# Kernel tuning notes

Hardware: AMD Instinct MI355X
Metric: run time of the kernel (lower is better)

The kernel has to match this reference:

```python
import jax, jax.numpy as jnp
import numpy as np

B, L, D, H = 8, 256, 512, 512
NEG_BIG = 1e8  # matches the 100000000.0 mask constant in the original


def setup_inputs() -> dict:
    key = jax.random.key(0)
    k1, k2, k3, k4 = jax.random.split(key, 4)
    enc = jax.random.normal(k1, (B, L, D), dtype=jnp.float32)
    # Glorot-uniform init, matching tf.keras.initializers.GlorotUniform
    s_w = float(np.sqrt(6.0 / (D + H)))
    W_l = jax.random.uniform(k2, (D, H), jnp.float32, -s_w, s_w)
    W_r = jax.random.uniform(k3, (D, H), jnp.float32, -s_w, s_w)
    s_u = float(np.sqrt(6.0 / (H + H)))  # 1-D glorot: fan_in = fan_out = H
    U = jax.random.uniform(k4, (H,), jnp.float32, -s_u, s_u)
    logit_bias = jnp.zeros((1,), jnp.float32)  # bias_initial_value=None -> zeros init
    return {"encoder_output": enc, "W_l": W_l, "W_r": W_r, "U": U, "logit_bias": logit_bias}


def reference(encoder_output, W_l, W_r, U, logit_bias):
    # dot_l[b,i,h], dot_r[b,j,h]
    dot_l = jnp.einsum('bik,kh->bih', encoder_output, W_l)
    dot_r = jnp.einsum('bjk,kh->bjh', encoder_output, W_r)
    # additive biaffine: tanh(dot_l_i + dot_r_j) . U  -> logits[b,i,j]
    final_sum = jnp.tanh(dot_l[:, :, None, :] + dot_r[:, None, :, :])  # [B,L,L,H]
    logits = jnp.einsum('bijh,h->bij', final_sum, U) + logit_bias[0]   # [B,L,L]
    # per-row self-mask (one_hot(i)) applied over all rows at once
    masked = logits - NEG_BIG * jnp.eye(L, dtype=logits.dtype)[None]   # [B,L,L]
    # original returns python lists over i of [B,L]; stack -> [L,B,L]
    mask_scores = jnp.transpose(masked, (1, 0, 2))
    p = jax.nn.sigmoid(mask_scores)
    samples = jax.random.bernoulli(jax.random.key(42), p).astype(jnp.int32)  # [L,B,L]
    # Bernoulli entropy from logits x: p*softplus(-x) + (1-p)*softplus(x)
    entropy = p * jax.nn.softplus(-mask_scores) + (1.0 - p) * jax.nn.softplus(mask_scores)
    return samples, mask_scores, entropy
```

## Files before the change

### kernel.cpp

```cpp
#include <hip/hip_runtime.h>
#include <stdint.h>

#define Bb 8
#define Ll 256
#define Dd 512
#define Hh 512
#define Nout (Ll * Bb * Ll)

#define Kc 2.8853900817779268

#define RNG_PARTITIONABLE 1

typedef __attribute__((ext_vector_type(8))) short bf16x8;
typedef __attribute__((ext_vector_type(4))) float f32x4;

__device__ __forceinline__ uint32_t rotl32(uint32_t v, int s) {
  return (v << s) | (v >> (32 - s));
}
__device__ __forceinline__ void tf_round(uint32_t& x0, uint32_t& x1, int r) {
  x0 += x1;
  x1 = rotl32(x1, r);
  x1 ^= x0;
}
__device__ __forceinline__ uint2 threefry2x32_k042(uint32_t x0, uint32_t x1) {
  const uint32_t k0 = 0u;
  const uint32_t k1 = 42u;
  const uint32_t k2 = 0x1BD11BDAu ^ k0 ^ k1;
  x0 += k0; x1 += k1;
  tf_round(x0, x1, 13); tf_round(x0, x1, 15); tf_round(x0, x1, 26); tf_round(x0, x1, 6);
  x0 += k1; x1 += k2 + 1u;
  tf_round(x0, x1, 17); tf_round(x0, x1, 29); tf_round(x0, x1, 16); tf_round(x0, x1, 24);
  x0 += k2; x1 += k0 + 2u;
  tf_round(x0, x1, 13); tf_round(x0, x1, 15); tf_round(x0, x1, 26); tf_round(x0, x1, 6);
  x0 += k0; x1 += k1 + 3u;
  tf_round(x0, x1, 17); tf_round(x0, x1, 29); tf_round(x0, x1, 16); tf_round(x0, x1, 24);
  x0 += k1; x1 += k2 + 4u;
  tf_round(x0, x1, 13); tf_round(x0, x1, 15); tf_round(x0, x1, 26); tf_round(x0, x1, 6);
  x0 += k2; x1 += k0 + 5u;
  return make_uint2(x0, x1);
}

__device__ __forceinline__ uint32_t rng_bits(uint32_t n) {
#if RNG_PARTITIONABLE
  uint2 o = threefry2x32_k042(0u, n);
  return o.x ^ o.y;
#else
  const uint32_t half = (uint32_t)(Nout / 2);
  if (n < half) {
    uint2 o = threefry2x32_k042(n, n + half);
    return o.x;
  } else {
    uint2 o = threefry2x32_k042(n - half, n);
    return o.y;
  }
#endif
}

__device__ __forceinline__ unsigned short bf16_rne(float f) {
  uint32_t u = __float_as_uint(f);
  u = (u + 0x7fffu + ((u >> 16) & 1u)) >> 16;
  return (unsigned short)u;
}
__device__ __forceinline__ float bf16_tof(unsigned short h) {
  return __uint_as_float(((uint32_t)h) << 16);
}
__device__ __forceinline__ void split3(float a, unsigned short& h,
                                       unsigned short& m, unsigned short& l) {
  h = bf16_rne(a);
  const float r1 = a - bf16_tof(h);
  m = bf16_rne(r1);
  const float r2 = r1 - bf16_tof(m);
  l = bf16_rne(r2);
}

__global__ __launch_bounds__(256) void split_enc(
    const float* __restrict__ enc, unsigned short* __restrict__ ah,
    unsigned short* __restrict__ am, unsigned short* __restrict__ al) {
  const int idx = (blockIdx.x * 256 + threadIdx.x) * 4;
  const float4 v = *(const float4*)(enc + idx);
  ushort4 h4, m4, l4;
  split3(v.x, h4.x, m4.x, l4.x);
  split3(v.y, h4.y, m4.y, l4.y);
  split3(v.z, h4.z, m4.z, l4.z);
  split3(v.w, h4.w, m4.w, l4.w);
  *(ushort4*)(ah + idx) = h4;
  *(ushort4*)(am + idx) = m4;
  *(ushort4*)(al + idx) = l4;
}

__global__ __launch_bounds__(256) void split_wt(
    const float* __restrict__ Wl, const float* __restrict__ Wr,
    unsigned short* __restrict__ wh, unsigned short* __restrict__ wm,
    unsigned short* __restrict__ wl) {
  const int z = blockIdx.z;
  const float* W = z ? Wr : Wl;
  const size_t zo = (size_t)z * Hh * Dd;
  const int k0 = blockIdx.x * 64;
  const int n0 = blockIdx.y * 64;
  __shared__ float tile[64][65];

  const int t = threadIdx.x;
#pragma unroll
  for (int rep = 0; rep < 4; ++rep) {
    const int idx = t + rep * 256;
    const int r = idx >> 4;
    const int c = (idx & 15) * 4;
    const float4 v = *(const float4*)(W + (size_t)(k0 + r) * Hh + n0 + c);
    tile[r][c + 0] = v.x; tile[r][c + 1] = v.y;
    tile[r][c + 2] = v.z; tile[r][c + 3] = v.w;
  }
  __syncthreads();
#pragma unroll
  for (int rep = 0; rep < 4; ++rep) {
    const int idx = t + rep * 256;
    const int rr = idx >> 4;
    const int cc = (idx & 15) * 4;
    ushort4 h4, m4, l4;
    split3(tile[cc + 0][rr], h4.x, m4.x, l4.x);
    split3(tile[cc + 1][rr], h4.y, m4.y, l4.y);
    split3(tile[cc + 2][rr], h4.z, m4.z, l4.z);
    split3(tile[cc + 3][rr], h4.w, m4.w, l4.w);
    const size_t o = zo + (size_t)(n0 + rr) * Dd + k0 + cc;
    *(ushort4*)(wh + o) = h4;
    *(ushort4*)(wm + o) = m4;
    *(ushort4*)(wl + o) = l4;
  }
}

__global__ __launch_bounds__(256) void gemm_mfma(
    const unsigned short* __restrict__ ah, const unsigned short* __restrict__ am,
    const unsigned short* __restrict__ al, const unsigned short* __restrict__ wh,
    const unsigned short* __restrict__ wm, const unsigned short* __restrict__ wl,
    float* __restrict__ el, float* __restrict__ er) {
  const int flat = blockIdx.x;
  const int xcd = flat & 7;
  const int loc = flat >> 3;
  const int z = loc >> 5;
  const int ni = (loc >> 2) & 7;
  const int mi = (xcd << 2) | (loc & 3);
  const size_t zo = (size_t)z * Hh * Dd;
  float* C = z ? er : el;
  const int m0 = mi * 64;
  const int n0 = ni * 64;

  __shared__ unsigned short Asm[2][12 * 512];
  __shared__ unsigned short Bsm[2][12 * 512];

  const int t = threadIdx.x;
  const int lane = t & 63;
  const int wv = t >> 6;
  const int l15 = lane & 15;
  const int kq8 = (lane >> 4) * 8;

  const unsigned short* gp[6];
  size_t go[6];
  int lq[6];
  bool isA[6];
#pragma unroll
  for (int s = 0; s < 6; ++s) {
    const int q = wv * 6 + s;
    if (q < 12) {
      const int p = q >> 2, mt = q & 3;
      gp[s] = (p == 0) ? ah : (p == 1) ? am : al;
      go[s] = (size_t)(m0 + mt * 16 + l15) * Dd + kq8;
      lq[s] = q * 512;
      isA[s] = true;
    } else {
      const int q2 = q - 12;
      const int p = q2 >> 2, nt = q2 & 3;
      gp[s] = (p == 0) ? wh : (p == 1) ? wm : wl;
      go[s] = zo + (size_t)(n0 + nt * 16 + l15) * Dd + kq8;
      lq[s] = q2 * 512;
      isA[s] = false;
    }
  }

  auto stage = [&](int buf, int kc) {
    const int k0 = kc * 32;
#pragma unroll
    for (int s = 0; s < 6; ++s) {
      unsigned short* dst = isA[s] ? &Asm[buf][lq[s]] : &Bsm[buf][lq[s]];
      __builtin_amdgcn_global_load_lds(
          (const __attribute__((address_space(1))) void*)(gp[s] + go[s] + k0),
          (__attribute__((address_space(3))) void*)dst, 16, 0, 0);
    }
  };

  const int mp = wv & 1;
  const int np = wv >> 1;

  f32x4 acc[2][2][2];
#pragma unroll
  for (int mi2 = 0; mi2 < 2; ++mi2)
#pragma unroll
    for (int ni2 = 0; ni2 < 2; ++ni2)
#pragma unroll
      for (int hf = 0; hf < 2; ++hf) acc[mi2][ni2][hf] = (f32x4){0.f, 0.f, 0.f, 0.f};

  stage(0, 0);
  __syncthreads();

  for (int kc = 0; kc < 16; ++kc) {
    const int buf = kc & 1;
    if (kc < 15) stage(buf ^ 1, kc + 1);

    bf16x8 af[2][3], bfr[2][3];
#pragma unroll
    for (int mi2 = 0; mi2 < 2; ++mi2)
#pragma unroll
      for (int p = 0; p < 3; ++p)
        af[mi2][p] = *(const bf16x8*)&Asm[buf][(p * 4 + mp * 2 + mi2) * 512 + lane * 8];
#pragma unroll
    for (int ni2 = 0; ni2 < 2; ++ni2)
#pragma unroll
      for (int p = 0; p < 3; ++p)
        bfr[ni2][p] = *(const bf16x8*)&Bsm[buf][(p * 4 + np * 2 + ni2) * 512 + lane * 8];

    const int hf = kc >> 3;
#pragma unroll
    for (int mi2 = 0; mi2 < 2; ++mi2)
#pragma unroll
      for (int ni2 = 0; ni2 < 2; ++ni2) {
        f32x4 A = acc[mi2][ni2][hf];
        A = __builtin_amdgcn_mfma_f32_16x16x32_bf16(af[mi2][0], bfr[ni2][0], A, 0, 0, 0);
        A = __builtin_amdgcn_mfma_f32_16x16x32_bf16(af[mi2][0], bfr[ni2][1], A, 0, 0, 0);
        A = __builtin_amdgcn_mfma_f32_16x16x32_bf16(af[mi2][1], bfr[ni2][0], A, 0, 0, 0);
        A = __builtin_amdgcn_mfma_f32_16x16x32_bf16(af[mi2][0], bfr[ni2][2], A, 0, 0, 0);
        A = __builtin_amdgcn_mfma_f32_16x16x32_bf16(af[mi2][2], bfr[ni2][0], A, 0, 0, 0);
        A = __builtin_amdgcn_mfma_f32_16x16x32_bf16(af[mi2][1], bfr[ni2][1], A, 0, 0, 0);
        acc[mi2][ni2][hf] = A;
      }
    __syncthreads();
  }

  const int rbase = (lane >> 4) * 4;
#pragma unroll
  for (int mi2 = 0; mi2 < 2; ++mi2) {
    const int mbase = m0 + (mp * 2 + mi2) * 16 + rbase;
#pragma unroll
    for (int ni2 = 0; ni2 < 2; ++ni2) {
      const int n = n0 + (np * 2 + ni2) * 16 + l15;
#pragma unroll
      for (int reg = 0; reg < 4; ++reg) {
        const double s = (double)acc[mi2][ni2][0][reg] + (double)acc[mi2][ni2][1][reg];
        C[(size_t)(mbase + reg) * Hh + n] = __builtin_amdgcn_exp2f((float)(Kc * s));
      }
    }
  }
}

__device__ __forceinline__ void group4_acc(float& S, const float4 a,
                                           const float4 bv, const float4 u) {
  const float d0 = __builtin_fmaf(a.x, bv.x, 1.0f);
  const float d1 = __builtin_fmaf(a.y, bv.y, 1.0f);
  const float d2 = __builtin_fmaf(a.z, bv.z, 1.0f);
  const float d3 = __builtin_fmaf(a.w, bv.w, 1.0f);
  const float p01 = d0 * d1;
  const float p23 = d2 * d3;
  const float D = p01 * p23;
  float n01 = u.x * d1;
  n01 = __builtin_fmaf(u.y, d0, n01);
  float n23 = u.z * d3;
  n23 = __builtin_fmaf(u.w, d2, n23);
  float num = n01 * p23;
  num = __builtin_fmaf(n23, p01, num);
  S = __builtin_fmaf(num, __builtin_amdgcn_rcpf(D), S);
}

__global__ __launch_bounds__(256) void biaffine_part(
    const float* __restrict__ el, const float* __restrict__ er,
    const float* __restrict__ U, float* __restrict__ part) {
  const int flat = blockIdx.x;
  const int b = flat & 7;
  const int loc = flat >> 3;
  const int ks = loc >> 4;
  const int ib = (loc >> 2) & 3;
  const int jb = loc & 3;
  const int i0 = ib * 64;
  const int j0 = jb * 64;
  const int h0 = ks * 64;

  __shared__ float els[64][68];
  __shared__ float ers[64][68];
  __shared__ float us[64];

  const int t = threadIdx.x;
  if (t < 16) *(float4*)&us[t * 4] = *(const float4*)(U + h0 + t * 4);

  const float* elg = el + (size_t)(b * Ll + i0) * Hh + h0;
  const float* erg = er + (size_t)(b * Ll + j0) * Hh + h0;
#pragma unroll
  for (int rep = 0; rep < 4; ++rep) {
    const int idx = t + rep * 256;
    const int r = idx >> 4;
    const int c = (idx & 15) * 4;
    *(float4*)&els[r][c] = *(const float4*)(elg + (size_t)r * Hh + c);
    *(float4*)&ers[r][c] = *(const float4*)(erg + (size_t)r * Hh + c);
  }
  __syncthreads();

  float usl = 0.0f;
#pragma unroll
  for (int q = 0; q < 16; ++q) {
    const float4 u = *(const float4*)&us[q * 4];
    usl += ((u.x + u.y) + u.z) + u.w;
  }

  const int ti = t >> 4;
  const int tj = t & 15;

  float S[4][4];
#pragma unroll
  for (int r = 0; r < 4; ++r)
#pragma unroll
    for (int c = 0; c < 4; ++c) S[r][c] = 0.0f;

  for (int g = 0; g < 16; ++g) {
    const int h = g * 4;
    const float4 u = *(const float4*)&us[h];
    float4 av[4], bv[4];
#pragma unroll
    for (int c = 0; c < 4; ++c) {
      av[c] = *(const float4*)&els[ti + 16 * c][h];
      bv[c] = *(const float4*)&ers[tj + 16 * c][h];
    }
#pragma unroll
    for (int r = 0; r < 4; ++r)
#pragma unroll
      for (int c = 0; c < 4; ++c) group4_acc(S[r][c], av[r], bv[c], u);
  }

  float* pslice = part + (size_t)ks * Nout;
#pragma unroll
  for (int r = 0; r < 4; ++r) {
    const int i = i0 + ti + 16 * r;
#pragma unroll
    for (int c = 0; c < 4; ++c) {
      const int j = j0 + tj + 16 * c;
      const uint32_t n = ((uint32_t)i * Bb + (uint32_t)b) * Ll + (uint32_t)j;
      pslice[n] = __builtin_fmaf(-2.0f, S[r][c], usl);
    }
  }
}

__global__ __launch_bounds__(256) void biaffine_emit(
    const float* __restrict__ part, const float* __restrict__ biasp,
    float* __restrict__ out) {
  const uint32_t n4 = (blockIdx.x * 256u + threadIdx.x) * 4u;
  double s0 = 0.0, s1 = 0.0, s2 = 0.0, s3 = 0.0;
#pragma unroll
  for (int k = 0; k < 8; ++k) {
    const float4 v = *(const float4*)(part + (size_t)k * Nout + n4);
    s0 += (double)v.x;
    s1 += (double)v.y;
    s2 += (double)v.z;
    s3 += (double)v.w;
  }
  const float bias = biasp[0];
  const double sv[4] = {s0, s1, s2, s3};

  float4 samp4, x4, ent4;
  float* sp = &samp4.x;
  float* xp = &x4.x;
  float* ep = &ent4.x;
#pragma unroll
  for (int q = 0; q < 4; ++q) {
    const uint32_t n = n4 + q;
    const int i = (int)(n >> 11);
    const int j = (int)(n & 255u);
    float x = (float)sv[q] + bias;
    if (i == j) x -= 1e8f;

    const double pd = 1.0 / (1.0 + exp(-(double)x));
    const float pf = (float)pd;

    const uint32_t bits = rng_bits(n);
    const float uu = __uint_as_float((bits >> 9) | 0x3f800000u) - 1.0f;
    sp[q] = (uu < pf) ? 1.0f : 0.0f;
    xp[q] = x;

    const float ax = fabsf(x);
    const float l1p = log1pf(expf(-ax));
    const float sp_pos = fmaxf(x, 0.0f) + l1p;
    const float sp_neg = fmaxf(-x, 0.0f) + l1p;
    ep[q] = pf * sp_neg + (1.0f - pf) * sp_pos;
  }
  *(float4*)(out + n4) = samp4;
  *(float4*)(out + Nout + n4) = x4;
  *(float4*)(out + 2 * (size_t)Nout + n4) = ent4;
}

extern "C" void kernel_launch(void* const* d_in, const int* in_sizes, int n_in,
                              void* d_out, int out_size, void* d_ws,
                              size_t ws_size, hipStream_t stream) {
  const float* enc = (const float*)d_in[0];
  const float* Wl = (const float*)d_in[1];
  const float* Wr = (const float*)d_in[2];
  const float* U = (const float*)d_in[3];
  const float* lb = (const float*)d_in[4];
  float* out = (float*)d_out;

  char* w = (char*)d_ws;
  float* el = (float*)w;                      w += (size_t)Bb * Ll * Hh * 4;
  float* er = (float*)w;                      w += (size_t)Bb * Ll * Hh * 4;
  float* part = (float*)w;                    w += (size_t)8 * Nout * 4;
  unsigned short* ah = (unsigned short*)w;    w += (size_t)Bb * Ll * Dd * 2;
  unsigned short* am = (unsigned short*)w;    w += (size_t)Bb * Ll * Dd * 2;
  unsigned short* al = (unsigned short*)w;    w += (size_t)Bb * Ll * Dd * 2;
  unsigned short* wh = (unsigned short*)w;    w += (size_t)2 * Dd * Hh * 2;
  unsigned short* wm = (unsigned short*)w;    w += (size_t)2 * Dd * Hh * 2;
  unsigned short* wl = (unsigned short*)w;    w += (size_t)2 * Dd * Hh * 2;

  split_enc<<<dim3((Bb * Ll * Dd) / 1024), 256, 0, stream>>>(enc, ah, am, al);
  split_wt<<<dim3(Dd / 64, Hh / 64, 2), 256, 0, stream>>>(Wl, Wr, wh, wm, wl);
  gemm_mfma<<<dim3(512, 1, 1), 256, 0, stream>>>(
      ah, am, al, wh, wm, wl, el, er);
  biaffine_part<<<dim3(1024, 1, 1), 256, 0, stream>>>(el, er, U, part);
  biaffine_emit<<<dim3(Nout / 1024), 256, 0, stream>>>(part, lb, out);
}
```

Baseline: 127.0 us.

## Merge split kernels, halve GEMM and biaffine tiles, remap partial-sum layout for XCD locality

The two bf16-split kernels become one launch with an XCD-aware block order. The GEMM N-tile shrinks from 64 to 32, doubling the block count. The biaffine_part i-tile halves to 32 rows, also doubling its grid. The partial-sum buffer is laid out batch-major so each batch's blocks stay on one XCD, and the emit kernel is remapped to read that layout. The aim is fewer launches, more blocks to fill CUs, and better L2 locality, at the cost of more redundant loads per output and uneven load counts per wave in the GEMM.

```diff
diff --git a/kernel.cpp b/kernel.cpp
--- a/kernel.cpp
+++ b/kernel.cpp
@@ -73,33 +73,41 @@
   l = bf16_rne(r2);
 }
 
-__global__ __launch_bounds__(256) void split_enc(
-    const float* __restrict__ enc, unsigned short* __restrict__ ah,
-    unsigned short* __restrict__ am, unsigned short* __restrict__ al) {
-  const int idx = (blockIdx.x * 256 + threadIdx.x) * 4;
-  const float4 v = *(const float4*)(enc + idx);
-  ushort4 h4, m4, l4;
-  split3(v.x, h4.x, m4.x, l4.x);
-  split3(v.y, h4.y, m4.y, l4.y);
-  split3(v.z, h4.z, m4.z, l4.z);
-  split3(v.w, h4.w, m4.w, l4.w);
-  *(ushort4*)(ah + idx) = h4;
-  *(ushort4*)(am + idx) = m4;
-  *(ushort4*)(al + idx) = l4;
-}
-
-__global__ __launch_bounds__(256) void split_wt(
-    const float* __restrict__ Wl, const float* __restrict__ Wr,
+__global__ __launch_bounds__(256) void split_all(
+    const float* __restrict__ enc, const float* __restrict__ Wl,
+    const float* __restrict__ Wr, unsigned short* __restrict__ ah,
+    unsigned short* __restrict__ am, unsigned short* __restrict__ al,
     unsigned short* __restrict__ wh, unsigned short* __restrict__ wm,
     unsigned short* __restrict__ wl) {
-  const int z = blockIdx.z;
+  __shared__ float tile[64][65];
+  const int bx = blockIdx.x;
+  const int t = threadIdx.x;
+
+  if (bx < 1024) {
+    const int d = ((bx & 7) << 7) | (bx >> 3);
+    const int idx = d * 1024 + t * 4;
+    const float4 v = *(const float4*)(enc + idx);
+    ushort4 h4, m4, l4;
+    split3(v.x, h4.x, m4.x, l4.x);
+    split3(v.y, h4.y, m4.y, l4.y);
+    split3(v.z, h4.z, m4.z, l4.z);
+    split3(v.w, h4.w, m4.w, l4.w);
+    *(ushort4*)(ah + idx) = h4;
+    *(ushort4*)(am + idx) = m4;
+    *(ushort4*)(al + idx) = l4;
+    return;
+  }
+
+  const int id = bx - 1024;
+  const int z = id >> 6;
+  const int rest = id & 63;
+  const int kb = rest >> 3;
+  const int nb = rest & 7;
   const float* W = z ? Wr : Wl;
   const size_t zo = (size_t)z * Hh * Dd;
-  const int k0 = blockIdx.x * 64;
-  const int n0 = blockIdx.y * 64;
-  __shared__ float tile[64][65];
-
-  const int t = threadIdx.x;
+  const int k0 = kb * 64;
+  const int n0 = nb * 64;
+
 #pragma unroll
   for (int rep = 0; rep < 4; ++rep) {
     const int idx = t + rep * 256;
@@ -135,16 +143,16 @@
   const int flat = blockIdx.x;
   const int xcd = flat & 7;
   const int loc = flat >> 3;
-  const int z = loc >> 5;
-  const int ni = (loc >> 2) & 7;
+  const int z = loc >> 6;
+  const int nblk = (loc >> 2) & 15;
   const int mi = (xcd << 2) | (loc & 3);
   const size_t zo = (size_t)z * Hh * Dd;
   float* C = z ? er : el;
   const int m0 = mi * 64;
-  const int n0 = ni * 64;
+  const int n0 = nblk * 32;
 
   __shared__ unsigned short Asm[2][12 * 512];
-  __shared__ unsigned short Bsm[2][12 * 512];
+  __shared__ unsigned short Bsm[2][6 * 512];
 
   const int t = threadIdx.x;
   const int lane = t & 63;
@@ -152,13 +160,15 @@
   const int l15 = lane & 15;
   const int kq8 = (lane >> 4) * 8;
 
-  const unsigned short* gp[6];
-  size_t go[6];
-  int lq[6];
-  bool isA[6];
-#pragma unroll
-  for (int s = 0; s < 6; ++s) {
-    const int q = wv * 6 + s;
+  const int nld = (wv < 2) ? 5 : 4;
+  const unsigned short* gp[5];
+  size_t go[5];
+  int lq[5];
+  bool isA[5];
+#pragma unroll
+  for (int s = 0; s < 5; ++s) {
+    int q = (wv < 2) ? (wv * 5 + s) : (10 + (wv - 2) * 4 + s);
+    if (q > 17) q = 17;
     if (q < 12) {
       const int p = q >> 2, mt = q & 3;
       gp[s] = (p == 0) ? ah : (p == 1) ? am : al;
@@ -167,7 +177,7 @@
       isA[s] = true;
     } else {
       const int q2 = q - 12;
-      const int p = q2 >> 2, nt = q2 & 3;
+      const int p = q2 >> 1, nt = q2 & 1;
       gp[s] = (p == 0) ? wh : (p == 1) ? wm : wl;
       go[s] = zo + (size_t)(n0 + nt * 16 + l15) * Dd + kq8;
       lq[s] = q2 * 512;
@@ -178,24 +188,24 @@
   auto stage = [&](int buf, int kc) {
     const int k0 = kc * 32;
 #pragma unroll
-    for (int s = 0; s < 6; ++s) {
-      unsigned short* dst = isA[s] ? &Asm[buf][lq[s]] : &Bsm[buf][lq[s]];
-      __builtin_amdgcn_global_load_lds(
-          (const __attribute__((address_space(1))) void*)(gp[s] + go[s] + k0),
-          (__attribute__((address_space(3))) void*)dst, 16, 0, 0);
+    for (int s = 0; s < 5; ++s) {
+      if (s < nld) {
+        unsigned short* dst = isA[s] ? &Asm[buf][lq[s]] : &Bsm[buf][lq[s]];
+        __builtin_amdgcn_global_load_lds(
+            (const __attribute__((address_space(1))) void*)(gp[s] + go[s] + k0),
+            (__attribute__((address_space(3))) void*)dst, 16, 0, 0);
+      }
     }
   };
 
   const int mp = wv & 1;
   const int np = wv >> 1;
 
-  f32x4 acc[2][2][2];
+  f32x4 acc[2][2];
 #pragma unroll
   for (int mi2 = 0; mi2 < 2; ++mi2)
 #pragma unroll
-    for (int ni2 = 0; ni2 < 2; ++ni2)
-#pragma unroll
-      for (int hf = 0; hf < 2; ++hf) acc[mi2][ni2][hf] = (f32x4){0.f, 0.f, 0.f, 0.f};
+    for (int hf = 0; hf < 2; ++hf) acc[mi2][hf] = (f32x4){0.f, 0.f, 0.f, 0.f};
 
   stage(0, 0);
   __syncthreads();
@@ -204,32 +214,28 @@
     const int buf = kc & 1;
     if (kc < 15) stage(buf ^ 1, kc + 1);
 
-    bf16x8 af[2][3], bfr[2][3];
+    bf16x8 af[2][3], bfr[3];
 #pragma unroll
     for (int mi2 = 0; mi2 < 2; ++mi2)
 #pragma unroll
       for (int p = 0; p < 3; ++p)
         af[mi2][p] = *(const bf16x8*)&Asm[buf][(p * 4 + mp * 2 + mi2) * 512 + lane * 8];
 #pragma unroll
-    for (int ni2 = 0; ni2 < 2; ++ni2)
-#pragma unroll
-      for (int p = 0; p < 3; ++p)
-        bfr[ni2][p] = *(const bf16x8*)&Bsm[buf][(p * 4 + np * 2 + ni2) * 512 + lane * 8];
+    for (int p = 0; p < 3; ++p)
+      bfr[p] = *(const bf16x8*)&Bsm[buf][(p * 2 + np) * 512 + lane * 8];
 
     const int hf = kc >> 3;
 #pragma unroll
-    for (int mi2 = 0; mi2 < 2; ++mi2)
-#pragma unroll
-      for (int ni2 = 0; ni2 < 2; ++ni2) {
-        f32x4 A = acc[mi2][ni2][hf];
-        A = __builtin_amdgcn_mfma_f32_16x16x32_bf16(af[mi2][0], bfr[ni2][0], A, 0, 0, 0);
-        A = __builtin_amdgcn_mfma_f32_16x16x32_bf16(af[mi2][0], bfr[ni2][1], A, 0, 0, 0);
-        A = __builtin_amdgcn_mfma_f32_16x16x32_bf16(af[mi2][1], bfr[ni2][0], A, 0, 0, 0);
-        A = __builtin_amdgcn_mfma_f32_16x16x32_bf16(af[mi2][0], bfr[ni2][2], A, 0, 0, 0);
-        A = __builtin_amdgcn_mfma_f32_16x16x32_bf16(af[mi2][2], bfr[ni2][0], A, 0, 0, 0);
-        A = __builtin_amdgcn_mfma_f32_16x16x32_bf16(af[mi2][1], bfr[ni2][1], A, 0, 0, 0);
-        acc[mi2][ni2][hf] = A;
-      }
+    for (int mi2 = 0; mi2 < 2; ++mi2) {
+      f32x4 A = acc[mi2][hf];
+      A = __builtin_amdgcn_mfma_f32_16x16x32_bf16(af[mi2][0], bfr[0], A, 0, 0, 0);
+      A = __builtin_amdgcn_mfma_f32_16x16x32_bf16(af[mi2][0], bfr[1], A, 0, 0, 0);
+      A = __builtin_amdgcn_mfma_f32_16x16x32_bf16(af[mi2][1], bfr[0], A, 0, 0, 0);
+      A = __builtin_amdgcn_mfma_f32_16x16x32_bf16(af[mi2][0], bfr[2], A, 0, 0, 0);
+      A = __builtin_amdgcn_mfma_f32_16x16x32_bf16(af[mi2][2], bfr[0], A, 0, 0, 0);
+      A = __builtin_amdgcn_mfma_f32_16x16x32_bf16(af[mi2][1], bfr[1], A, 0, 0, 0);
+      acc[mi2][hf] = A;
+    }
     __syncthreads();
   }
 
@@ -237,14 +243,11 @@
 #pragma unroll
   for (int mi2 = 0; mi2 < 2; ++mi2) {
     const int mbase = m0 + (mp * 2 + mi2) * 16 + rbase;
-#pragma unroll
-    for (int ni2 = 0; ni2 < 2; ++ni2) {
-      const int n = n0 + (np * 2 + ni2) * 16 + l15;
-#pragma unroll
-      for (int reg = 0; reg < 4; ++reg) {
-        const double s = (double)acc[mi2][ni2][0][reg] + (double)acc[mi2][ni2][1][reg];
-        C[(size_t)(mbase + reg) * Hh + n] = __builtin_amdgcn_exp2f((float)(Kc * s));
-      }
+    const int n = n0 + np * 16 + l15;
+#pragma unroll
+    for (int reg = 0; reg < 4; ++reg) {
+      const double s = (double)acc[mi2][0][reg] + (double)acc[mi2][1][reg];
+      C[(size_t)(mbase + reg) * Hh + n] = __builtin_amdgcn_exp2f((float)(Kc * s));
     }
   }
 }
@@ -273,14 +276,14 @@
   const int flat = blockIdx.x;
   const int b = flat & 7;
   const int loc = flat >> 3;
-  const int ks = loc >> 4;
-  const int ib = (loc >> 2) & 3;
+  const int ks = loc >> 5;
+  const int ib = (loc >> 2) & 7;
   const int jb = loc & 3;
-  const int i0 = ib * 64;
+  const int i0 = ib * 32;
   const int j0 = jb * 64;
   const int h0 = ks * 64;
 
-  __shared__ float els[64][68];
+  __shared__ float els[32][68];
   __shared__ float ers[64][68];
   __shared__ float us[64];
 
@@ -289,13 +292,16 @@
 
   const float* elg = el + (size_t)(b * Ll + i0) * Hh + h0;
   const float* erg = er + (size_t)(b * Ll + j0) * Hh + h0;
-#pragma unroll
-  for (int rep = 0; rep < 4; ++rep) {
-    const int idx = t + rep * 256;
-    const int r = idx >> 4;
-    const int c = (idx & 15) * 4;
-    *(float4*)&els[r][c] = *(const float4*)(elg + (size_t)r * Hh + c);
-    *(float4*)&ers[r][c] = *(const float4*)(erg + (size_t)r * Hh + c);
+  {
+    const int r0 = t >> 4;
+    const int c = (t & 15) * 4;
+    *(float4*)&els[r0][c] = *(const float4*)(elg + (size_t)r0 * Hh + c);
+    *(float4*)&els[r0 + 16][c] = *(const float4*)(elg + (size_t)(r0 + 16) * Hh + c);
+#pragma unroll
+    for (int rep = 0; rep < 4; ++rep) {
+      const int r = (t + rep * 256) >> 4;
+      *(float4*)&ers[r][c] = *(const float4*)(erg + (size_t)r * Hh + c);
+    }
   }
   __syncthreads();
 
@@ -309,36 +315,35 @@
   const int ti = t >> 4;
   const int tj = t & 15;
 
-  float S[4][4];
-#pragma unroll
-  for (int r = 0; r < 4; ++r)
+  float S[2][4];
+#pragma unroll
+  for (int r = 0; r < 2; ++r)
 #pragma unroll
     for (int c = 0; c < 4; ++c) S[r][c] = 0.0f;
 
   for (int g = 0; g < 16; ++g) {
     const int h = g * 4;
     const float4 u = *(const float4*)&us[h];
-    float4 av[4], bv[4];
-#pragma unroll
-    for (int c = 0; c < 4; ++c) {
-      av[c] = *(const float4*)&els[ti + 16 * c][h];
-      bv[c] = *(const float4*)&ers[tj + 16 * c][h];
-    }
-#pragma unroll
-    for (int r = 0; r < 4; ++r)
+    float4 av[2], bv[4];
+#pragma unroll
+    for (int r = 0; r < 2; ++r) av[r] = *(const float4*)&els[ti + 16 * r][h];
+#pragma unroll
+    for (int c = 0; c < 4; ++c) bv[c] = *(const float4*)&ers[tj + 16 * c][h];
+#pragma unroll
+    for (int r = 0; r < 2; ++r)
 #pragma unroll
       for (int c = 0; c < 4; ++c) group4_acc(S[r][c], av[r], bv[c], u);
   }
 
   float* pslice = part + (size_t)ks * Nout;
 #pragma unroll
-  for (int r = 0; r < 4; ++r) {
+  for (int r = 0; r < 2; ++r) {
     const int i = i0 + ti + 16 * r;
 #pragma unroll
     for (int c = 0; c < 4; ++c) {
       const int j = j0 + tj + 16 * c;
-      const uint32_t n = ((uint32_t)i * Bb + (uint32_t)b) * Ll + (uint32_t)j;
-      pslice[n] = __builtin_fmaf(-2.0f, S[r][c], usl);
+      const uint32_t m = ((uint32_t)b << 16) | ((uint32_t)i << 8) | (uint32_t)j;
+      pslice[m] = __builtin_fmaf(-2.0f, S[r][c], usl);
     }
   }
 }
@@ -346,11 +351,16 @@
 __global__ __launch_bounds__(256) void biaffine_emit(
     const float* __restrict__ part, const float* __restrict__ biasp,
     float* __restrict__ out) {
-  const uint32_t n4 = (blockIdx.x * 256u + threadIdx.x) * 4u;
+  const int flat = blockIdx.x;
+  const int b = flat & 7;
+  const int loc = flat >> 3;
+  const uint32_t mi4 = (uint32_t)loc * 1024u + (uint32_t)threadIdx.x * 4u;
+  const uint32_t mbase = ((uint32_t)b << 16) | mi4;
+
   double s0 = 0.0, s1 = 0.0, s2 = 0.0, s3 = 0.0;
 #pragma unroll
   for (int k = 0; k < 8; ++k) {
-    const float4 v = *(const float4*)(part + (size_t)k * Nout + n4);
+    const float4 v = *(const float4*)(part + (size_t)k * Nout + mbase);
     s0 += (double)v.x;
     s1 += (double)v.y;
     s2 += (double)v.z;
@@ -359,15 +369,18 @@
   const float bias = biasp[0];
   const double sv[4] = {s0, s1, s2, s3};
 
+  const int i = (int)(mi4 >> 8);
+  const int jb = (int)(mi4 & 255u);
+  const uint32_t nb = (((uint32_t)i * Bb + (uint32_t)b) << 8) | (uint32_t)jb;
+
   float4 samp4, x4, ent4;
   float* sp = &samp4.x;
   float* xp = &x4.x;
   float* ep = &ent4.x;
 #pragma unroll
   for (int q = 0; q < 4; ++q) {
-    const uint32_t n = n4 + q;
-    const int i = (int)(n >> 11);
-    const int j = (int)(n & 255u);
+    const uint32_t n = nb + q;
+    const int j = jb + q;
     float x = (float)sv[q] + bias;
     if (i == j) x -= 1e8f;
 
@@ -385,9 +398,9 @@
     const float sp_neg = fmaxf(-x, 0.0f) + l1p;
     ep[q] = pf * sp_neg + (1.0f - pf) * sp_pos;
   }
-  *(float4*)(out + n4) = samp4;
-  *(float4*)(out + Nout + n4) = x4;
-  *(float4*)(out + 2 * (size_t)Nout + n4) = ent4;
+  *(float4*)(out + nb) = samp4;
+  *(float4*)(out + Nout + nb) = x4;
+  *(float4*)(out + 2 * (size_t)Nout + nb) = ent4;
 }
 
 extern "C" void kernel_launch(void* const* d_in, const int* in_sizes, int n_in,
@@ -411,10 +424,10 @@
   unsigned short* wm = (unsigned short*)w;    w += (size_t)2 * Dd * Hh * 2;
   unsigned short* wl = (unsigned short*)w;    w += (size_t)2 * Dd * Hh * 2;
 
-  split_enc<<<dim3((Bb * Ll * Dd) / 1024), 256, 0, stream>>>(enc, ah, am, al);
-  split_wt<<<dim3(Dd / 64, Hh / 64, 2), 256, 0, stream>>>(Wl, Wr, wh, wm, wl);
-  gemm_mfma<<<dim3(512, 1, 1), 256, 0, stream>>>(
+  split_all<<<dim3(1024 + 128), 256, 0, stream>>>(enc, Wl, Wr, ah, am, al,
+                                                  wh, wm, wl);
+  gemm_mfma<<<dim3(1024, 1, 1), 256, 0, stream>>>(
       ah, am, al, wh, wm, wl, el, er);
-  biaffine_part<<<dim3(1024, 1, 1), 256, 0, stream>>>(el, er, U, part);
-  biaffine_emit<<<dim3(Nout / 1024), 256, 0, stream>>>(part, lb, out);
-}
+  biaffine_part<<<dim3(2048, 1, 1), 256, 0, stream>>>(el, er, U, part);
+  biaffine_emit<<<dim3(512, 1, 1), 256, 0, stream>>>(part, lb, out);
+}
```

New measurement: 141.9 us. 11.8% more time.
